# Kernel optimization log

Hardware: AMD Instinct MI355X
Metric: run time of the kernel (lower is better)

Reference implementation:

```python
import jax, jax.numpy as jnp
import numpy as np

B, M, K, N = 4, 2048, 4096, 4096


def setup_inputs() -> dict:
    key = jax.random.key(0)
    k1, k2, k3, k4, k5 = jax.random.split(key, 5)
    # int8 quantized activations and weights (stored as int8, like the torch buffers)
    x_q = jax.random.randint(k1, (B, M, K), -128, 127, dtype=jnp.int8)
    weight = jax.random.randint(k2, (N, K), -128, 127, dtype=jnp.int8)
    # per-token activation scales and per-output-row weight scales (symmetric quant)
    scales_x = jax.random.uniform(k3, (B, M, 1), dtype=jnp.float32) * 0.01 + 1e-4
    weight_scales = jax.random.uniform(k4, (N, 1), dtype=jnp.float32) * 0.01 + 1e-4
    bias = jax.random.normal(k5, (N,), dtype=jnp.float32)
    return {"x_q": x_q, "scales_x": scales_x, "weight": weight,
            "weight_scales": weight_scales, "bias": bias}


def reference(x_q, scales_x, weight, weight_scales, bias):
    # int8 GEMM accumulating in int32: (B*M, K) @ (K, N) with weight stored (N, K)
    acc = jnp.einsum(
        'bmk,nk->bmn',
        x_q.astype(jnp.int32), weight.astype(jnp.int32),
        preferred_element_type=jnp.int32,
    )  # [B, M, N] int32
    # symmetric dequant: row (token) scale * column (output-channel) scale, then bias
    out = acc.astype(jnp.float32) * scales_x * weight_scales[:, 0] + bias
    return out.astype(jnp.float16)
```

## Files before the change

kernel.cpp:

```cpp
#include <hip/hip_runtime.h>

typedef int v4i __attribute__((ext_vector_type(4)));

constexpr int Kdim = 4096;
constexpr int Ndim = 4096;
constexpr int MtotC = 8192;
constexpr int BM = 256;
constexpr int BN = 256;
constexpr int BKB = 128;
constexpr int NT = Kdim / BKB;

__global__ void pack_i32_to_i8(const int* __restrict__ xq, const int* __restrict__ wq,
                               signed char* __restrict__ x8, signed char* __restrict__ w8,
                               size_t nx4, size_t nw4) {
    size_t i = (size_t)blockIdx.x * blockDim.x + threadIdx.x;
    size_t stride = (size_t)gridDim.x * blockDim.x;
    size_t tot = nx4 + nw4;
    for (size_t j = i; j < tot; j += stride) {
        if (j < nx4) {
            const int4 v = ((const int4*)xq)[j];
            char4 c;
            c.x = (signed char)v.x; c.y = (signed char)v.y;
            c.z = (signed char)v.z; c.w = (signed char)v.w;
            ((char4*)x8)[j] = c;
        } else {
            const size_t k = j - nx4;
            const int4 v = ((const int4*)wq)[k];
            char4 c;
            c.x = (signed char)v.x; c.y = (signed char)v.y;
            c.z = (signed char)v.z; c.w = (signed char)v.w;
            ((char4*)w8)[k] = c;
        }
    }
}

__global__ __launch_bounds__(512, 2) void i8gemm_kernel(
    const signed char* __restrict__ A,
    const signed char* __restrict__ W,
    const float* __restrict__ sx,
    const float* __restrict__ wsc,
    const float* __restrict__ bias,
    float* __restrict__ C)
{
    extern __shared__ signed char smem[];

    const int tid  = threadIdx.x;
    const int wave = tid >> 6;
    const int lane = tid & 63;
    const int wr = wave >> 2;
    const int wc = wave & 3;

    const int xr_ = blockIdx.x & 7;
    const int idx = blockIdx.x >> 3;
    const int bm = ((xr_ & 3) * 8 + (idx & 7)) * BM;
    const int bn = ((xr_ >> 2) * 8 + (idx >> 3)) * BN;

    const int srow_in = wave * 16 + (lane >> 2);
    const int sslotp  = lane & 3;
    const int gslot   = sslotp ^ ((srow_in >> 1) & 3);
    const signed char* Ag = A + (size_t)(bm + srow_in) * Kdim + gslot * 16;
    const signed char* Wg = W + (size_t)(bn + srow_in) * Kdim + gslot * 16;
    const int sdst = srow_in * 64 + sslotp * 16;

    const int frow = lane & 15;
    const int fsl  = lane >> 4;
    const int rsw  = ((fsl ^ ((frow >> 1) & 3)) << 4);
    const int aro  = (wr * 128 + frow) * 64 + rsw;
    const int bro  = 16384 + (wc * 64 + frow) * 64 + rsw;

    v4i acc[8][4];
#pragma unroll
    for (int f = 0; f < 8; ++f)
#pragma unroll
        for (int g = 0; g < 4; ++g)
#pragma unroll
            for (int e = 0; e < 4; ++e) acc[f][g][e] = 0;

#define STG(KT, HALF, RB) do {                                                         \
    __builtin_amdgcn_global_load_lds(                                                  \
        (const __attribute__((address_space(1))) void*)(Ag + (size_t)(RB) * Kdim + (KT) * BKB + (HALF) * 64), \
        (__attribute__((address_space(3))) void*)(smem + ((KT) & 1) * 65536 + (HALF) * 32768 + (RB) * 64 + sdst), \
        16, 0, 0);                                                                     \
    __builtin_amdgcn_global_load_lds(                                                  \
        (const __attribute__((address_space(1))) void*)(Wg + (size_t)(RB) * Kdim + (KT) * BKB + (HALF) * 64), \
        (__attribute__((address_space(3))) void*)(smem + ((KT) & 1) * 65536 + (HALF) * 32768 + 16384 + (RB) * 64 + sdst), \
        16, 0, 0);                                                                     \
} while (0)

#define STAGEFULL(KT) do {                                                             \
    STG(KT, 0, 0);  STG(KT, 0, 128);                                                   \
    STG(KT, 1, 0);  STG(KT, 1, 128);                                                   \
} while (0)

#define BAR __builtin_amdgcn_s_barrier()

    STAGEFULL(0);
    STAGEFULL(1);
    asm volatile("s_waitcnt vmcnt(8)" ::: "memory");
    BAR;

    for (int u = 0; u < NT; ++u) {
        const signed char* bufb = smem + (u & 1) * 65536;

        v4i av0[8], bv0[4], av1[8], bv1[4];
#pragma unroll
        for (int g = 0; g < 4; ++g) bv0[g] = *(const v4i*)(bufb + bro + g * 1024);
#pragma unroll
        for (int f = 0; f < 8; ++f) av0[f] = *(const v4i*)(bufb + aro + f * 1024);
#pragma unroll
        for (int g = 0; g < 4; ++g) bv1[g] = *(const v4i*)(bufb + 32768 + bro + g * 1024);
#pragma unroll
        for (int f = 0; f < 8; ++f) av1[f] = *(const v4i*)(bufb + 32768 + aro + f * 1024);

#pragma unroll
        for (int f = 0; f < 8; ++f)
#pragma unroll
            for (int g = 0; g < 4; ++g)
                acc[f][g] = __builtin_amdgcn_mfma_i32_16x16x64_i8(av0[f], bv0[g], acc[f][g], 0, 0, 0);
#pragma unroll
        for (int f = 0; f < 8; ++f)
#pragma unroll
            for (int g = 0; g < 4; ++g)
                acc[f][g] = __builtin_amdgcn_mfma_i32_16x16x64_i8(av1[f], bv1[g], acc[f][g], 0, 0, 0);

        BAR;

        if (u + 2 < NT) {
            STAGEFULL(u + 2);
            asm volatile("s_waitcnt vmcnt(8)" ::: "memory");
            BAR;
        } else if (u + 1 < NT) {
            asm volatile("s_waitcnt vmcnt(0)" ::: "memory");
            BAR;
        }
    }

    const int orow0 = bm + wr * 128;
    const int ocol0 = bn + wc * 64;
    float wsv[4], bvv[4];
#pragma unroll
    for (int g = 0; g < 4; ++g) {
        const int col = ocol0 + g * 16 + frow;
        wsv[g] = wsc[col];
        bvv[g] = bias[col];
    }
#pragma unroll
    for (int f = 0; f < 8; ++f) {
#pragma unroll
        for (int jr = 0; jr < 4; ++jr) {
            const int row = orow0 + f * 16 + fsl * 4 + jr;
            const float s = sx[row];
#pragma unroll
            for (int g = 0; g < 4; ++g) {
                const int col = ocol0 + g * 16 + frow;
                C[(size_t)row * Ndim + col] = (float)acc[f][g][jr] * s * wsv[g] + bvv[g];
            }
        }
    }
#undef STG
#undef STAGEFULL
#undef BAR
}

extern "C" void kernel_launch(void* const* d_in, const int* in_sizes, int n_in,
                              void* d_out, int out_size, void* d_ws, size_t ws_size,
                              hipStream_t stream) {
    (void)in_sizes; (void)n_in; (void)out_size; (void)ws_size;
    const int*   x_q  = (const int*)d_in[0];
    const float* sx   = (const float*)d_in[1];
    const int*   w_q  = (const int*)d_in[2];
    const float* wsc  = (const float*)d_in[3];
    const float* bias = (const float*)d_in[4];
    float* out = (float*)d_out;

    signed char* x8 = (signed char*)d_ws;
    signed char* w8 = x8 + (size_t)MtotC * Kdim;

    const size_t nx = (size_t)MtotC * Kdim;
    const size_t nw = (size_t)Ndim * Kdim;

    pack_i32_to_i8<<<3072, 256, 0, stream>>>(x_q, w_q, x8, w8, nx / 4, nw / 4);

    static bool attr_set = false;
    if (!attr_set) {
        hipFuncSetAttribute((const void*)i8gemm_kernel,
                            hipFuncAttributeMaxDynamicSharedMemorySize, 131072);
        attr_set = true;
    }

    const int nwg = (MtotC / BM) * (Ndim / BN);
    i8gemm_kernel<<<nwg, 512, 131072, stream>>>(x8, w8, sx, wsc, bias, out);
}
```

Baseline: 190.6 us.

## Shrink GEMM tile to 128x256x64 with 4 waves and static LDS

Retiles the int8 GEMM from 256x256 tiles with a K-step of 128 and 8 waves to 128x256 tiles with a K-step of 64 and 4 waves, each wave computing 64x128. Static shared memory drops from 128KB to 48KB double-buffered, which should allow more workgroups per CU and doubles the number of workgroups for better load balance. It also raises wave priority around the MFMA block and remaps the XCD block swizzle. The costs are lower arithmetic intensity per tile, more global traffic for W, and twice as many barrier iterations.

New measurement: 203.4 us. +6.7%, slower.

```diff
diff --git a/kernel.cpp b/kernel.cpp
--- a/kernel.cpp
+++ b/kernel.cpp
@@ -5,9 +5,9 @@
 constexpr int Kdim = 4096;
 constexpr int Ndim = 4096;
 constexpr int MtotC = 8192;
-constexpr int BM = 256;
+constexpr int BM = 128;
 constexpr int BN = 256;
-constexpr int BKB = 128;
+constexpr int BKB = 64;
 constexpr int NT = Kdim / BKB;
 
 __global__ void pack_i32_to_i8(const int* __restrict__ xq, const int* __restrict__ wq,
@@ -34,7 +34,7 @@
     }
 }
 
-__global__ __launch_bounds__(512, 2) void i8gemm_kernel(
+__global__ __launch_bounds__(256, 2) void i8gemm_kernel(
     const signed char* __restrict__ A,
     const signed char* __restrict__ W,
     const float* __restrict__ sx,
@@ -42,92 +42,80 @@
     const float* __restrict__ bias,
     float* __restrict__ C)
 {
-    extern __shared__ signed char smem[];
+    __shared__ signed char smem[2][24576];
 
     const int tid  = threadIdx.x;
     const int wave = tid >> 6;
     const int lane = tid & 63;
-    const int wr = wave >> 2;
-    const int wc = wave & 3;
+    const int wr = wave >> 1;
+    const int wc = wave & 1;
 
-    const int xr_ = blockIdx.x & 7;
+    const int xcd = blockIdx.x & 7;
     const int idx = blockIdx.x >> 3;
-    const int bm = ((xr_ & 3) * 8 + (idx & 7)) * BM;
-    const int bn = ((xr_ >> 2) * 8 + (idx >> 3)) * BN;
+    const int bm = ((xcd & 3) * 16 + (idx & 15)) * BM;
+    const int bn = ((xcd >> 2) * 8 + (idx >> 4)) * BN;
 
-    const int srow_in = wave * 16 + (lane >> 2);
-    const int sslotp  = lane & 3;
-    const int gslot   = sslotp ^ ((srow_in >> 1) & 3);
-    const signed char* Ag = A + (size_t)(bm + srow_in) * Kdim + gslot * 16;
-    const signed char* Wg = W + (size_t)(bn + srow_in) * Kdim + gslot * 16;
-    const int sdst = srow_in * 64 + sslotp * 16;
+    const int srow4 = tid >> 2;
+    const int gslot = (tid & 3) ^ ((tid >> 3) & 3);
+    const signed char* Ag = A + (size_t)(bm + srow4) * Kdim + gslot * 16;
+    const signed char* Wg = W + (size_t)(bn + srow4) * Kdim + gslot * 16;
 
     const int frow = lane & 15;
     const int fsl  = lane >> 4;
     const int rsw  = ((fsl ^ ((frow >> 1) & 3)) << 4);
-    const int aro  = (wr * 128 + frow) * 64 + rsw;
-    const int bro  = 16384 + (wc * 64 + frow) * 64 + rsw;
+    const int aro  = (wr * 64 + frow) * 64 + rsw;
+    const int bro  = 8192 + (wc * 128 + frow) * 64 + rsw;
 
-    v4i acc[8][4];
+    v4i acc[4][8];
 #pragma unroll
-    for (int f = 0; f < 8; ++f)
+    for (int f = 0; f < 4; ++f)
 #pragma unroll
-        for (int g = 0; g < 4; ++g)
+        for (int g = 0; g < 8; ++g)
 #pragma unroll
             for (int e = 0; e < 4; ++e) acc[f][g][e] = 0;
 
-#define STG(KT, HALF, RB) do {                                                         \
-    __builtin_amdgcn_global_load_lds(                                                  \
-        (const __attribute__((address_space(1))) void*)(Ag + (size_t)(RB) * Kdim + (KT) * BKB + (HALF) * 64), \
-        (__attribute__((address_space(3))) void*)(smem + ((KT) & 1) * 65536 + (HALF) * 32768 + (RB) * 64 + sdst), \
-        16, 0, 0);                                                                     \
-    __builtin_amdgcn_global_load_lds(                                                  \
-        (const __attribute__((address_space(1))) void*)(Wg + (size_t)(RB) * Kdim + (KT) * BKB + (HALF) * 64), \
-        (__attribute__((address_space(3))) void*)(smem + ((KT) & 1) * 65536 + (HALF) * 32768 + 16384 + (RB) * 64 + sdst), \
-        16, 0, 0);                                                                     \
-} while (0)
-
-#define STAGEFULL(KT) do {                                                             \
-    STG(KT, 0, 0);  STG(KT, 0, 128);                                                   \
-    STG(KT, 1, 0);  STG(KT, 1, 128);                                                   \
+#define STG(KT) do {                                                                   \
+    signed char* dst = &smem[(KT) & 1][0];                                             \
+    const size_t ko = (size_t)(KT) * BKB;                                              \
+    _Pragma("unroll") for (int r = 0; r < 2; ++r)                                      \
+        __builtin_amdgcn_global_load_lds(                                              \
+            (const __attribute__((address_space(1))) void*)(Ag + (size_t)(r * 64) * Kdim + ko), \
+            (__attribute__((address_space(3))) void*)(dst + r * 4096 + tid * 16), 16, 0, 0);    \
+    _Pragma("unroll") for (int rb = 0; rb < 4; ++rb)                                   \
+        __builtin_amdgcn_global_load_lds(                                              \
+            (const __attribute__((address_space(1))) void*)(Wg + (size_t)(rb * 64) * Kdim + ko), \
+            (__attribute__((address_space(3))) void*)(dst + 8192 + rb * 4096 + tid * 16), 16, 0, 0); \
 } while (0)
 
 #define BAR __builtin_amdgcn_s_barrier()
 
-    STAGEFULL(0);
-    STAGEFULL(1);
-    asm volatile("s_waitcnt vmcnt(8)" ::: "memory");
+    STG(0);
+    STG(1);
+    asm volatile("s_waitcnt vmcnt(6)" ::: "memory");
     BAR;
 
     for (int u = 0; u < NT; ++u) {
-        const signed char* bufb = smem + (u & 1) * 65536;
+        const signed char* bufb = &smem[u & 1][0];
 
-        v4i av0[8], bv0[4], av1[8], bv1[4];
+        v4i av[4], bv[8];
 #pragma unroll
-        for (int g = 0; g < 4; ++g) bv0[g] = *(const v4i*)(bufb + bro + g * 1024);
+        for (int g = 0; g < 8; ++g) bv[g] = *(const v4i*)(bufb + bro + g * 1024);
 #pragma unroll
-        for (int f = 0; f < 8; ++f) av0[f] = *(const v4i*)(bufb + aro + f * 1024);
+        for (int f = 0; f < 4; ++f) av[f] = *(const v4i*)(bufb + aro + f * 1024);
+
+        __builtin_amdgcn_s_setprio(1);
 #pragma unroll
-        for (int g = 0; g < 4; ++g) bv1[g] = *(const v4i*)(bufb + 32768 + bro + g * 1024);
+        for (int f = 0; f < 4; ++f)
 #pragma unroll
-        for (int f = 0; f < 8; ++f) av1[f] = *(const v4i*)(bufb + 32768 + aro + f * 1024);
-
-#pragma unroll
-        for (int f = 0; f < 8; ++f)
-#pragma unroll
-            for (int g = 0; g < 4; ++g)
-                acc[f][g] = __builtin_amdgcn_mfma_i32_16x16x64_i8(av0[f], bv0[g], acc[f][g], 0, 0, 0);
-#pragma unroll
-        for (int f = 0; f < 8; ++f)
-#pragma unroll
-            for (int g = 0; g < 4; ++g)
-                acc[f][g] = __builtin_amdgcn_mfma_i32_16x16x64_i8(av1[f], bv1[g], acc[f][g], 0, 0, 0);
+            for (int g = 0; g < 8; ++g)
+                acc[f][g] = __builtin_amdgcn_mfma_i32_16x16x64_i8(av[f], bv[g], acc[f][g], 0, 0, 0);
+        __builtin_amdgcn_s_setprio(0);
 
         BAR;
 
         if (u + 2 < NT) {
-            STAGEFULL(u + 2);
-            asm volatile("s_waitcnt vmcnt(8)" ::: "memory");
+            STG(u + 2);
+            asm volatile("s_waitcnt vmcnt(6)" ::: "memory");
             BAR;
         } else if (u + 1 < NT) {
             asm volatile("s_waitcnt vmcnt(0)" ::: "memory");
@@ -135,30 +123,29 @@
         }
     }
 
-    const int orow0 = bm + wr * 128;
-    const int ocol0 = bn + wc * 64;
-    float wsv[4], bvv[4];
+    const int orow0 = bm + wr * 64;
+    const int ocol0 = bn + wc * 128;
+    float wsv[8], bvv[8];
 #pragma unroll
-    for (int g = 0; g < 4; ++g) {
+    for (int g = 0; g < 8; ++g) {
         const int col = ocol0 + g * 16 + frow;
         wsv[g] = wsc[col];
         bvv[g] = bias[col];
     }
 #pragma unroll
-    for (int f = 0; f < 8; ++f) {
+    for (int f = 0; f < 4; ++f) {
 #pragma unroll
         for (int jr = 0; jr < 4; ++jr) {
             const int row = orow0 + f * 16 + fsl * 4 + jr;
             const float s = sx[row];
 #pragma unroll
-            for (int g = 0; g < 4; ++g) {
+            for (int g = 0; g < 8; ++g) {
                 const int col = ocol0 + g * 16 + frow;
                 C[(size_t)row * Ndim + col] = (float)acc[f][g][jr] * s * wsv[g] + bvv[g];
             }
         }
     }
 #undef STG
-#undef STAGEFULL
 #undef BAR
 }
 
@@ -181,13 +168,6 @@
 
     pack_i32_to_i8<<<3072, 256, 0, stream>>>(x_q, w_q, x8, w8, nx / 4, nw / 4);
 
-    static bool attr_set = false;
-    if (!attr_set) {
-        hipFuncSetAttribute((const void*)i8gemm_kernel,
-                            hipFuncAttributeMaxDynamicSharedMemorySize, 131072);
-        attr_set = true;
-    }
-
     const int nwg = (MtotC / BM) * (Ndim / BN);
-    i8gemm_kernel<<<nwg, 512, 131072, stream>>>(x8, w8, sx, wsc, bias, out);
+    i8gemm_kernel<<<nwg, 256, 0, stream>>>(x8, w8, sx, wsc, bias, out);
 }
```

## Use 4 waves per block with 128x128 per-wave tiles instead of 8 waves

Applied to the files above, without the earlier changes.

Halves the threads per 256x256 block from 512 to 256, so each wave computes a 128x128 output tile (8x8 MFMA fragments) rather than 128x64. The aim is more MFMA work per LDS fragment read and fewer waves competing for LDS bandwidth. Staging is rewritten so each thread issues 16 async global-to-LDS loads per K-tile. Accumulator registers double to 256 per lane, which removes wave-level latency hiding and may cause register spills.

Result: slower. 253.2 us (+32.8%).

```diff
diff --git a/kernel.cpp b/kernel.cpp
--- a/kernel.cpp
+++ b/kernel.cpp
@@ -34,7 +34,7 @@
     }
 }
 
-__global__ __launch_bounds__(512, 2) void i8gemm_kernel(
+__global__ __launch_bounds__(256, 1) void i8gemm_kernel(
     const signed char* __restrict__ A,
     const signed char* __restrict__ W,
     const float* __restrict__ sx,
@@ -47,87 +47,84 @@
     const int tid  = threadIdx.x;
     const int wave = tid >> 6;
     const int lane = tid & 63;
-    const int wr = wave >> 2;
-    const int wc = wave & 3;
+    const int wr = wave >> 1;
+    const int wc = wave & 1;
 
     const int xr_ = blockIdx.x & 7;
     const int idx = blockIdx.x >> 3;
     const int bm = ((xr_ & 3) * 8 + (idx & 7)) * BM;
     const int bn = ((xr_ >> 2) * 8 + (idx >> 3)) * BN;
 
-    const int srow_in = wave * 16 + (lane >> 2);
-    const int sslotp  = lane & 3;
-    const int gslot   = sslotp ^ ((srow_in >> 1) & 3);
-    const signed char* Ag = A + (size_t)(bm + srow_in) * Kdim + gslot * 16;
-    const signed char* Wg = W + (size_t)(bn + srow_in) * Kdim + gslot * 16;
-    const int sdst = srow_in * 64 + sslotp * 16;
+    const int srow = tid >> 2;
+    const int gslot = (tid & 3) ^ ((tid >> 3) & 3);
+    const signed char* Ag = A + (size_t)(bm + srow) * Kdim + gslot * 16;
+    const signed char* Wg = W + (size_t)(bn + srow) * Kdim + gslot * 16;
 
     const int frow = lane & 15;
     const int fsl  = lane >> 4;
     const int rsw  = ((fsl ^ ((frow >> 1) & 3)) << 4);
     const int aro  = (wr * 128 + frow) * 64 + rsw;
-    const int bro  = 16384 + (wc * 64 + frow) * 64 + rsw;
+    const int bro  = 16384 + (wc * 128 + frow) * 64 + rsw;
 
-    v4i acc[8][4];
+    v4i acc[8][8];
 #pragma unroll
     for (int f = 0; f < 8; ++f)
 #pragma unroll
-        for (int g = 0; g < 4; ++g)
+        for (int g = 0; g < 8; ++g)
 #pragma unroll
             for (int e = 0; e < 4; ++e) acc[f][g][e] = 0;
 
-#define STG(KT, HALF, RB) do {                                                         \
-    __builtin_amdgcn_global_load_lds(                                                  \
-        (const __attribute__((address_space(1))) void*)(Ag + (size_t)(RB) * Kdim + (KT) * BKB + (HALF) * 64), \
-        (__attribute__((address_space(3))) void*)(smem + ((KT) & 1) * 65536 + (HALF) * 32768 + (RB) * 64 + sdst), \
-        16, 0, 0);                                                                     \
-    __builtin_amdgcn_global_load_lds(                                                  \
-        (const __attribute__((address_space(1))) void*)(Wg + (size_t)(RB) * Kdim + (KT) * BKB + (HALF) * 64), \
-        (__attribute__((address_space(3))) void*)(smem + ((KT) & 1) * 65536 + (HALF) * 32768 + 16384 + (RB) * 64 + sdst), \
-        16, 0, 0);                                                                     \
-} while (0)
-
-#define STAGEFULL(KT) do {                                                             \
-    STG(KT, 0, 0);  STG(KT, 0, 128);                                                   \
-    STG(KT, 1, 0);  STG(KT, 1, 128);                                                   \
+#define STG(KT) do {                                                                   \
+    signed char* dst = smem + ((KT) & 1) * 65536;                                      \
+    const size_t ko = (size_t)(KT) * BKB;                                              \
+    _Pragma("unroll") for (int h = 0; h < 2; ++h) {                                    \
+        _Pragma("unroll") for (int r = 0; r < 4; ++r)                                  \
+            __builtin_amdgcn_global_load_lds(                                          \
+                (const __attribute__((address_space(1))) void*)(Ag + (size_t)(r * 64) * Kdim + ko + h * 64), \
+                (__attribute__((address_space(3))) void*)(dst + h * 32768 + r * 4096 + tid * 16), 16, 0, 0); \
+        _Pragma("unroll") for (int r = 0; r < 4; ++r)                                  \
+            __builtin_amdgcn_global_load_lds(                                          \
+                (const __attribute__((address_space(1))) void*)(Wg + (size_t)(r * 64) * Kdim + ko + h * 64), \
+                (__attribute__((address_space(3))) void*)(dst + h * 32768 + 16384 + r * 4096 + tid * 16), 16, 0, 0); \
+    }                                                                                  \
 } while (0)
 
 #define BAR __builtin_amdgcn_s_barrier()
 
-    STAGEFULL(0);
-    STAGEFULL(1);
-    asm volatile("s_waitcnt vmcnt(8)" ::: "memory");
+    STG(0);
+    STG(1);
+    asm volatile("s_waitcnt vmcnt(16)" ::: "memory");
     BAR;
 
     for (int u = 0; u < NT; ++u) {
         const signed char* bufb = smem + (u & 1) * 65536;
 
-        v4i av0[8], bv0[4], av1[8], bv1[4];
+        v4i av0[8], bv0[8], av1[8], bv1[8];
 #pragma unroll
-        for (int g = 0; g < 4; ++g) bv0[g] = *(const v4i*)(bufb + bro + g * 1024);
+        for (int g = 0; g < 8; ++g) bv0[g] = *(const v4i*)(bufb + bro + g * 1024);
 #pragma unroll
         for (int f = 0; f < 8; ++f) av0[f] = *(const v4i*)(bufb + aro + f * 1024);
 #pragma unroll
-        for (int g = 0; g < 4; ++g) bv1[g] = *(const v4i*)(bufb + 32768 + bro + g * 1024);
+        for (int g = 0; g < 8; ++g) bv1[g] = *(const v4i*)(bufb + 32768 + bro + g * 1024);
 #pragma unroll
         for (int f = 0; f < 8; ++f) av1[f] = *(const v4i*)(bufb + 32768 + aro + f * 1024);
 
 #pragma unroll
         for (int f = 0; f < 8; ++f)
 #pragma unroll
-            for (int g = 0; g < 4; ++g)
+            for (int g = 0; g < 8; ++g)
                 acc[f][g] = __builtin_amdgcn_mfma_i32_16x16x64_i8(av0[f], bv0[g], acc[f][g], 0, 0, 0);
 #pragma unroll
         for (int f = 0; f < 8; ++f)
 #pragma unroll
-            for (int g = 0; g < 4; ++g)
+            for (int g = 0; g < 8; ++g)
                 acc[f][g] = __builtin_amdgcn_mfma_i32_16x16x64_i8(av1[f], bv1[g], acc[f][g], 0, 0, 0);
 
         BAR;
 
         if (u + 2 < NT) {
-            STAGEFULL(u + 2);
-            asm volatile("s_waitcnt vmcnt(8)" ::: "memory");
+            STG(u + 2);
+            asm volatile("s_waitcnt vmcnt(16)" ::: "memory");
             BAR;
         } else if (u + 1 < NT) {
             asm volatile("s_waitcnt vmcnt(0)" ::: "memory");
@@ -136,10 +133,10 @@
     }
 
     const int orow0 = bm + wr * 128;
-    const int ocol0 = bn + wc * 64;
-    float wsv[4], bvv[4];
+    const int ocol0 = bn + wc * 128;
+    float wsv[8], bvv[8];
 #pragma unroll
-    for (int g = 0; g < 4; ++g) {
+    for (int g = 0; g < 8; ++g) {
         const int col = ocol0 + g * 16 + frow;
         wsv[g] = wsc[col];
         bvv[g] = bias[col];
@@ -151,14 +148,13 @@
             const int row = orow0 + f * 16 + fsl * 4 + jr;
             const float s = sx[row];
 #pragma unroll
-            for (int g = 0; g < 4; ++g) {
+            for (int g = 0; g < 8; ++g) {
                 const int col = ocol0 + g * 16 + frow;
                 C[(size_t)row * Ndim + col] = (float)acc[f][g][jr] * s * wsv[g] + bvv[g];
             }
         }
     }
 #undef STG
-#undef STAGEFULL
 #undef BAR
 }
 
@@ -189,5 +185,5 @@
     }
 
     const int nwg = (MtotC / BM) * (Ndim / BN);
-    i8gemm_kernel<<<nwg, 512, 131072, stream>>>(x8, w8, sx, wsc, bias, out);
+    i8gemm_kernel<<<nwg, 256, 131072, stream>>>(x8, w8, sx, wsc, bias, out);
 }
```

## Load B fragments directly into registers, stage only A through LDS

Applied to the files above, without the earlier changes.

The weight (B) operand is no longer staged through shared memory. Each wave now loads its B fragments straight from global memory into registers, prefetching the next half-tile while the MFMAs run, and only A is double-buffered in LDS. This halves LDS footprint to 64KB static, which could allow more occupancy, and cuts LDS traffic and the B staging loads. The loop is also restructured into a macro with s_setprio around MFMA blocks and sched barriers. The risk is that B global loads are redundant across the wr wave rows and can stall the MFMAs if the prefetch latency is not hidden.

New measurement: 217.3 us. 14.0% more time.

```diff
diff --git a/kernel.cpp b/kernel.cpp
--- a/kernel.cpp
+++ b/kernel.cpp
@@ -42,7 +42,7 @@
     const float* __restrict__ bias,
     float* __restrict__ C)
 {
-    extern __shared__ signed char smem[];
+    __shared__ signed char smem[65536];
 
     const int tid  = threadIdx.x;
     const int wave = tid >> 6;
@@ -55,18 +55,16 @@
     const int bm = ((xr_ & 3) * 8 + (idx & 7)) * BM;
     const int bn = ((xr_ >> 2) * 8 + (idx >> 3)) * BN;
 
-    const int srow_in = wave * 16 + (lane >> 2);
-    const int sslotp  = lane & 3;
-    const int gslot   = sslotp ^ ((srow_in >> 1) & 3);
-    const signed char* Ag = A + (size_t)(bm + srow_in) * Kdim + gslot * 16;
-    const signed char* Wg = W + (size_t)(bn + srow_in) * Kdim + gslot * 16;
-    const int sdst = srow_in * 64 + sslotp * 16;
+    const int srow  = tid >> 2;
+    const int gslot = (tid & 3) ^ ((srow >> 1) & 3);
+    const signed char* Ag = A + (size_t)(bm + srow) * Kdim + gslot * 16;
 
     const int frow = lane & 15;
     const int fsl  = lane >> 4;
     const int rsw  = ((fsl ^ ((frow >> 1) & 3)) << 4);
     const int aro  = (wr * 128 + frow) * 64 + rsw;
-    const int bro  = 16384 + (wc * 64 + frow) * 64 + rsw;
+
+    const signed char* Bg = W + (size_t)(bn + wc * 64 + frow) * Kdim + fsl * 16;
 
     v4i acc[8][4];
 #pragma unroll
@@ -76,64 +74,76 @@
 #pragma unroll
             for (int e = 0; e < 4; ++e) acc[f][g][e] = 0;
 
-#define STG(KT, HALF, RB) do {                                                         \
-    __builtin_amdgcn_global_load_lds(                                                  \
-        (const __attribute__((address_space(1))) void*)(Ag + (size_t)(RB) * Kdim + (KT) * BKB + (HALF) * 64), \
-        (__attribute__((address_space(3))) void*)(smem + ((KT) & 1) * 65536 + (HALF) * 32768 + (RB) * 64 + sdst), \
-        16, 0, 0);                                                                     \
-    __builtin_amdgcn_global_load_lds(                                                  \
-        (const __attribute__((address_space(1))) void*)(Wg + (size_t)(RB) * Kdim + (KT) * BKB + (HALF) * 64), \
-        (__attribute__((address_space(3))) void*)(smem + ((KT) & 1) * 65536 + (HALF) * 32768 + 16384 + (RB) * 64 + sdst), \
-        16, 0, 0);                                                                     \
-} while (0)
+    v4i bh0[4], bh1[4];
 
-#define STAGEFULL(KT) do {                                                             \
-    STG(KT, 0, 0);  STG(KT, 0, 128);                                                   \
-    STG(KT, 1, 0);  STG(KT, 1, 128);                                                   \
+#define STG_A(KT) do {                                                                 \
+    signed char* dst = smem + ((KT) & 1) * 32768 + tid * 16;                           \
+    const size_t ko = (size_t)(KT) * BKB;                                              \
+    _Pragma("unroll") for (int h = 0; h < 2; ++h)                                      \
+    _Pragma("unroll") for (int r = 0; r < 2; ++r)                                      \
+        __builtin_amdgcn_global_load_lds(                                              \
+            (const __attribute__((address_space(1))) void*)(Ag + (size_t)(r * 128) * Kdim + ko + h * 64), \
+            (__attribute__((address_space(3))) void*)(dst + h * 16384 + r * 8192), 16, 0, 0); \
 } while (0)
 
 #define BAR __builtin_amdgcn_s_barrier()
 
-    STAGEFULL(0);
-    STAGEFULL(1);
-    asm volatile("s_waitcnt vmcnt(8)" ::: "memory");
+#pragma unroll
+    for (int g = 0; g < 4; ++g) bh0[g] = *(const v4i*)(Bg + g * 65536);
+    STG_A(0);
+    STG_A(1);
+    asm volatile("s_waitcnt vmcnt(4)" ::: "memory");
     BAR;
 
-    for (int u = 0; u < NT; ++u) {
-        const signed char* bufb = smem + (u & 1) * 65536;
+#define TILE(U, DOB0, DOS, DOTAIL) do {                                                \
+    const signed char* bufb = smem + ((U) & 1) * 32768;                                \
+                            \
+    _Pragma("unroll") for (int g = 0; g < 4; ++g)                                      \
+        bh1[g] = *(const v4i*)(Bg + g * 65536 + (U) * 128 + 64);                       \
+                                                   \
+    {                                                                                  \
+        v4i av[8];                                                                     \
+        _Pragma("unroll") for (int f = 0; f < 8; ++f)                                  \
+            av[f] = *(const v4i*)(bufb + aro + f * 1024);                              \
+        __builtin_amdgcn_s_setprio(1);                                                 \
+        _Pragma("unroll") for (int f = 0; f < 8; ++f)                                  \
+        _Pragma("unroll") for (int g = 0; g < 4; ++g)                                  \
+            acc[f][g] = __builtin_amdgcn_mfma_i32_16x16x64_i8(av[f], bh0[g], acc[f][g], 0, 0, 0); \
+        __builtin_amdgcn_s_setprio(0);                                                 \
+    }                                                                                  \
+    __builtin_amdgcn_sched_barrier(0);                                                 \
+                              \
+    if (DOB0) {                                                                        \
+        _Pragma("unroll") for (int g = 0; g < 4; ++g)                                  \
+            bh0[g] = *(const v4i*)(Bg + g * 65536 + ((U) + 1) * 128);                  \
+    }                                                                                  \
+                                                   \
+    {                                                                                  \
+        v4i av[8];                                                                     \
+        _Pragma("unroll") for (int f = 0; f < 8; ++f)                                  \
+            av[f] = *(const v4i*)(bufb + 16384 + aro + f * 1024);                      \
+        __builtin_amdgcn_s_setprio(1);                                                 \
+        _Pragma("unroll") for (int f = 0; f < 8; ++f)                                  \
+        _Pragma("unroll") for (int g = 0; g < 4; ++g)                                  \
+            acc[f][g] = __builtin_amdgcn_mfma_i32_16x16x64_i8(av[f], bh1[g], acc[f][g], 0, 0, 0); \
+        __builtin_amdgcn_s_setprio(0);                                                 \
+    }                                                                                  \
+    if (DOTAIL) {                                                                      \
+        BAR;                                                                           \
+        if (DOS) {                                                                     \
+            STG_A((U) + 2);                                                            \
+            asm volatile("s_waitcnt vmcnt(4)" ::: "memory");        \
+        } else {                                                                       \
+            asm volatile("s_waitcnt vmcnt(0)" ::: "memory");                           \
+        }                                                                              \
+        BAR;                                                                           \
+    }                                                                                  \
+} while (0)
 
-        v4i av0[8], bv0[4], av1[8], bv1[4];
-#pragma unroll
-        for (int g = 0; g < 4; ++g) bv0[g] = *(const v4i*)(bufb + bro + g * 1024);
-#pragma unroll
-        for (int f = 0; f < 8; ++f) av0[f] = *(const v4i*)(bufb + aro + f * 1024);
-#pragma unroll
-        for (int g = 0; g < 4; ++g) bv1[g] = *(const v4i*)(bufb + 32768 + bro + g * 1024);
-#pragma unroll
-        for (int f = 0; f < 8; ++f) av1[f] = *(const v4i*)(bufb + 32768 + aro + f * 1024);
-
-#pragma unroll
-        for (int f = 0; f < 8; ++f)
-#pragma unroll
-            for (int g = 0; g < 4; ++g)
-                acc[f][g] = __builtin_amdgcn_mfma_i32_16x16x64_i8(av0[f], bv0[g], acc[f][g], 0, 0, 0);
-#pragma unroll
-        for (int f = 0; f < 8; ++f)
-#pragma unroll
-            for (int g = 0; g < 4; ++g)
-                acc[f][g] = __builtin_amdgcn_mfma_i32_16x16x64_i8(av1[f], bv1[g], acc[f][g], 0, 0, 0);
-
-        BAR;
-
-        if (u + 2 < NT) {
-            STAGEFULL(u + 2);
-            asm volatile("s_waitcnt vmcnt(8)" ::: "memory");
-            BAR;
-        } else if (u + 1 < NT) {
-            asm volatile("s_waitcnt vmcnt(0)" ::: "memory");
-            BAR;
-        }
-    }
+    for (int u = 0; u < NT - 2; ++u)
+        TILE(u, true, true, true);
+    TILE(NT - 2, true, false, true);
+    TILE(NT - 1, false, false, false);
 
     const int orow0 = bm + wr * 128;
     const int ocol0 = bn + wc * 64;
@@ -157,9 +167,9 @@
             }
         }
     }
-#undef STG
-#undef STAGEFULL
+#undef STG_A
 #undef BAR
+#undef TILE
 }
 
 extern "C" void kernel_launch(void* const* d_in, const int* in_sizes, int n_in,
@@ -181,13 +191,6 @@
 
     pack_i32_to_i8<<<3072, 256, 0, stream>>>(x_q, w_q, x8, w8, nx / 4, nw / 4);
 
-    static bool attr_set = false;
-    if (!attr_set) {
-        hipFuncSetAttribute((const void*)i8gemm_kernel,
-                            hipFuncAttributeMaxDynamicSharedMemorySize, 131072);
-        attr_set = true;
-    }
-
     const int nwg = (MtotC / BM) * (Ndim / BN);
-    i8gemm_kernel<<<nwg, 512, 131072, stream>>>(x8, w8, sx, wsc, bias, out);
+    i8gemm_kernel<<<nwg, 512, 0, stream>>>(x8, w8, sx, wsc, bias, out);
 }
```
